# Kernel tuning notes

Measured on AMD Instinct MI355X. Metric: run time of the kernel, lower is better.

Reference implementation:

```python
import jax, jax.numpy as jnp
import numpy as np

EPS = 1e-7
CAPS_N = 1152   # 32 maps * 6 * 6
CAPS1_DIM = 8
CAPS2_N = 10
CAPS2_DIM = 16


def squash(s, axis):
    sq = jnp.sum(jnp.square(s), axis=axis, keepdims=True)
    norm = jnp.sqrt(sq + EPS)
    return (sq / (1.0 + sq)) * (s / norm)


def _conv(x, k, b, stride):
    y = jax.lax.conv_general_dilated(x, k, (stride, stride), 'VALID',
                                     dimension_numbers=('NHWC', 'HWIO', 'NHWC'))
    return jax.nn.relu(y + b)


def setup_inputs() -> dict:
    key = jax.random.key(0)
    ks = jax.random.split(key, 8)
    B = 256
    return {
        'image': jax.random.uniform(ks[0], (B, 28, 28, 1), dtype=jnp.float32),
        'target': jax.random.randint(ks[1], (B,), 0, CAPS2_N),
        'conv1_w': jax.random.normal(ks[2], (9, 9, 1, 256), jnp.float32) * 0.05,
        'conv1_b': jnp.zeros((256,), jnp.float32),
        'conv2_w': jax.random.normal(ks[3], (9, 9, 256, 256), jnp.float32) * 0.02,
        'conv2_b': jnp.zeros((256,), jnp.float32),
        'W': jax.random.normal(ks[4], (1, CAPS_N, CAPS2_N, CAPS2_DIM, CAPS1_DIM), jnp.float32) * 0.1,
        'd1_w': jax.random.normal(ks[5], (CAPS2_N * CAPS2_DIM, 512), jnp.float32) * 0.05,
        'd1_b': jnp.zeros((512,), jnp.float32),
        'd2_w': jax.random.normal(ks[6], (512, 1024), jnp.float32) * 0.04,
        'd2_b': jnp.zeros((1024,), jnp.float32),
        'd3_w': jax.random.normal(ks[7], (1024, 784), jnp.float32) * 0.03,
        'd3_b': jnp.zeros((784,), jnp.float32),
    }


def reference(image, target, conv1_w, conv1_b, conv2_w, conv2_b, W,
              d1_w, d1_b, d2_w, d2_b, d3_w, d3_b):
    B = image.shape[0]
    h = _conv(image, conv1_w, conv1_b, 1)        # [B,20,20,256]
    h = _conv(h, conv2_w, conv2_b, 2)            # [B,6,6,256]
    pc = squash(h.reshape(B, CAPS_N, CAPS1_DIM), axis=-1)  # [B,1152,8]
    # u_hat[b,n,c,j] = sum_i W[0,n,c,j,i] * pc[b,n,i]  (avoids explicit tiling)
    u_hat = jnp.einsum('ncji,bni->bncj', W[0], pc)          # [B,1152,10,16]
    # round 1: softmax of zeros over the 10 digit caps == uniform 1/10
    s1 = jnp.sum(u_hat, axis=1) * (1.0 / CAPS2_N)           # [B,10,16]
    v1 = squash(s1, axis=-1)
    # agreement uv[b,n,c] = <u_hat[b,n,c,:], v1[b,c,:]>
    uv = jnp.einsum('bncj,bcj->bnc', u_hat, v1)             # [B,1152,10]
    # round 2
    c2 = jax.nn.softmax(uv, axis=2)
    s2 = jnp.einsum('bnc,bncj->bcj', c2, u_hat)             # [B,10,16]
    v2 = squash(s2, axis=-1)                                # [B,10,16]
    norm_v2 = jnp.sqrt(jnp.sum(jnp.square(v2), axis=-1, keepdims=True) + EPS)
    norm_v2 = norm_v2[:, None, :, :, None]                  # [B,1,10,1,1]
    y_pred = jnp.squeeze(jnp.argmax(norm_v2, axis=2), axis=(1, 2))  # [B,1]
    # training path: mask by target one-hot
    mask = jax.nn.one_hot(target, CAPS2_N, dtype=v2.dtype)  # [B,10]
    masked = v2 * mask[:, :, None]                          # [B,10,16]
    flat = masked.reshape(B, 1, CAPS2_N * CAPS2_DIM)        # [B,1,160]
    h1 = jax.nn.relu(flat @ d1_w + d1_b)
    h2 = jax.nn.relu(h1 @ d2_w + d2_b)
    dec = jax.nn.sigmoid(h2 @ d3_w + d3_b)                  # [B,1,784]
    return norm_v2, y_pred, dec
```

## Files before the change

### kernel.cpp

```cpp
#include <hip/hip_runtime.h>
#include <math.h>

#define EPS 1e-7f
#define IN1_ELEMS 26214400
#define BT_ELEMS  5308416

typedef float fvec4 __attribute__((ext_vector_type(4)));
typedef short short8 __attribute__((ext_vector_type(8)));
typedef __bf16 bf16x8 __attribute__((ext_vector_type(8)));

__device__ inline unsigned short f2bf(float f){
  unsigned int u = __float_as_uint(f);
  unsigned int r = (u + 0x7fffu + ((u >> 16) & 1u)) >> 16;
  return (unsigned short)r;
}
__device__ inline float bf2f(unsigned short h){
  return __uint_as_float(((unsigned int)h) << 16);
}
__device__ inline void async16(unsigned short* dst, const unsigned short* src){
  __builtin_amdgcn_global_load_lds((const __attribute__((address_space(1))) void*)src,
                                   (__attribute__((address_space(3))) void*)dst, 16, 0, 0);
}
__device__ inline fvec4 mfma_bf16(short8 a, short8 b, fvec4 c){
  return __builtin_amdgcn_mfma_f32_16x16x32_bf16(
      __builtin_bit_cast(bf16x8, a), __builtin_bit_cast(bf16x8, b), c, 0, 0, 0);
}

__global__ __launch_bounds__(256) void wt_kernel(const float* __restrict__ w2,
    unsigned short* __restrict__ BTh, unsigned short* __restrict__ BTl){
  __shared__ float tile[64][65];
  int t = threadIdx.x;
  int k0 = blockIdx.x * 64, oc0 = blockIdx.y * 64;
  #pragma unroll
  for (int p = 0; p < 16; ++p){
    int f = p*256 + t;
    int kr = f >> 6, cc = f & 63;
    tile[kr][cc] = w2[(size_t)(k0 + kr)*256 + oc0 + cc];
  }
  __syncthreads();
  #pragma unroll
  for (int p = 0; p < 16; ++p){
    int f = p*256 + t;
    int ocr = f >> 6, kc = f & 63;
    float v = tile[kc][ocr];
    unsigned short h = f2bf(v);
    size_t idx = (size_t)(oc0 + ocr)*20736 + k0 + kc;
    BTh[idx] = h;
    BTl[idx] = f2bf(v - bf2f(h));
  }
}

__global__ __launch_bounds__(256) void conv1_kernel(const float* __restrict__ img,
    const float* __restrict__ w1, const float* __restrict__ b1,
    unsigned short* __restrict__ outh, unsigned short* __restrict__ outl){
  __shared__ float sim[252];
  int t = threadIdx.x;
  int oh = blockIdx.x, b = blockIdx.y;
  if (t < 252) sim[t] = img[((size_t)b*28 + oh + t/28)*28 + (t%28)];
  __syncthreads();
  float acc[20];
  #pragma unroll
  for (int i = 0; i < 20; ++i) acc[i] = 0.f;
  #pragma unroll
  for (int kh = 0; kh < 9; ++kh){
    float im[28];
    #pragma unroll
    for (int c = 0; c < 28; ++c) im[c] = sim[kh*28 + c];
    #pragma unroll
    for (int kw = 0; kw < 9; ++kw){
      float wv = w1[(kh*9 + kw)*256 + t];
      #pragma unroll
      for (int ow = 0; ow < 20; ++ow) acc[ow] = fmaf(im[ow + kw], wv, acc[ow]);
    }
  }
  float bv = b1[t];
  size_t base = ((size_t)(b*20 + oh))*20*256 + t;
  #pragma unroll
  for (int ow = 0; ow < 20; ++ow){
    float v = fmaxf(acc[ow] + bv, 0.f);
    unsigned short h = f2bf(v);
    outh[base + ow*256] = h;
    outl[base + ow*256] = f2bf(v - bf2f(h));
  }
}

__global__ __launch_bounds__(256) void conv2_mfma(const unsigned short* __restrict__ in1h,
    const unsigned short* __restrict__ BTh, float* __restrict__ out){
  __shared__ __align__(16) unsigned short lds[16384];
  const int t = threadIdx.x;
  const int lane = t & 63, w = t >> 6;
  const int m0 = blockIdx.y * 128, n0 = blockIdx.x * 128;
  const int rowA = t >> 2, seg = t & 3;

  const unsigned short* aS[2];
  const unsigned short* bS[2];
  #pragma unroll
  for (int h = 0; h < 2; ++h){
    int m = m0 + h*64 + rowA;
    int bb = m / 36, s = m - bb*36, oh = s / 6, ow = s - oh*6;
    aS[h] = in1h + ((size_t)((bb*20 + 2*oh)*20 + 2*ow))*256 + seg*8;
    int n = n0 + h*64 + rowA;
    bS[h] = BTh + (size_t)n*20736 + seg*8;
  }
  unsigned short* dstA = &lds[rowA*32 + seg*8];
  unsigned short* dstB = &lds[8192 + rowA*32 + seg*8];

  fvec4 acc[4][4];
  #pragma unroll
  for (int i=0;i<4;++i)
    #pragma unroll
    for (int j=0;j<4;++j) acc[i][j] = (fvec4){0.f,0.f,0.f,0.f};

  const int qm = (w >> 1)*64, qn = (w & 1)*64;
  const int ks0 = blockIdx.z * 81, ks1 = ks0 + 81;

  for (int ks = ks0; ks < ks1; ++ks){
    int kk = ks >> 3;
    int kh = kk / 9, kw = kk - kh*9;
    int aoff = (kh*20 + kw)*256 + (ks & 7)*32;
    int boff = ks*32;
    #pragma unroll
    for (int h = 0; h < 2; ++h){
      async16(dstA + h*2048,        aS[h] + aoff);
      async16(dstA + 4096 + h*2048, aS[h] + IN1_ELEMS + aoff);
      async16(dstB + h*2048,        bS[h] + boff);
      async16(dstB + 4096 + h*2048, bS[h] + BT_ELEMS + boff);
    }
    __syncthreads();
    short8 ah[4], al[4], bh[4], bl[4];
    #pragma unroll
    for (int i=0;i<4;++i){
      int ro = (qm + i*16 + (lane & 15))*32 + (lane >> 4)*8;
      ah[i] = *(const short8*)&lds[ro];
      al[i] = *(const short8*)&lds[4096 + ro];
    }
    #pragma unroll
    for (int j=0;j<4;++j){
      int ro = (qn + j*16 + (lane & 15))*32 + (lane >> 4)*8;
      bh[j] = *(const short8*)&lds[8192 + ro];
      bl[j] = *(const short8*)&lds[12288 + ro];
    }
    #pragma unroll
    for (int i=0;i<4;++i)
      #pragma unroll
      for (int j=0;j<4;++j){
        acc[i][j] = mfma_bf16(ah[i], bh[j], acc[i][j]);
        acc[i][j] = mfma_bf16(ah[i], bl[j], acc[i][j]);
        acc[i][j] = mfma_bf16(al[i], bh[j], acc[i][j]);
      }
    __syncthreads();
  }
  #pragma unroll
  for (int i=0;i<4;++i){
    int gm = m0 + qm + i*16 + ((lane >> 4) << 2);
    #pragma unroll
    for (int j=0;j<4;++j){
      int gn = n0 + qn + j*16 + (lane & 15);
      #pragma unroll
      for (int r=0;r<4;++r)
        atomicAdd(&out[(size_t)(gm + r)*256 + gn], acc[i][j][r]);
    }
  }
}

__global__ __launch_bounds__(256) void squash_pc_kernel(const float* __restrict__ c2out,
    const float* __restrict__ b2, float* __restrict__ pc){
  int g = blockIdx.x*256 + threadIdx.x;
  const float* s = c2out + (size_t)g*8;
  int oc0 = (g & 31) * 8;
  float v[8], sq = 0.f;
  #pragma unroll
  for (int e=0;e<8;++e){ float x = fmaxf(s[e] + b2[oc0+e], 0.f); v[e] = x; sq += x*x; }
  float fac = sq / ((1.f + sq) * sqrtf(sq + EPS));
  float* o = pc + (size_t)g*8;
  #pragma unroll
  for (int e=0;e<8;++e) o[e] = v[e]*fac;
}

__global__ __launch_bounds__(256) void uhat_producer(const float* __restrict__ pc,
    const float* __restrict__ Wm, float* __restrict__ uhat, float* __restrict__ s1){
  __shared__ float pcl[8192];
  int t = threadIdx.x;
  int n0 = blockIdx.x * 16, b0 = blockIdx.y * 64;
  #pragma unroll
  for (int p = 0; p < 32; ++p){
    int f = p*256 + t;
    int bl = f >> 7, rem = f & 127;
    pcl[f] = pc[((size_t)(b0 + bl)*1152 + n0)*8 + rem];
  }
  __syncthreads();
  for (int r = 0; r < 40; ++r){
    int item = r*256 + t;
    int bl = item / 160, cj = item - bl*160;
    float s1a = 0.f;
    size_t ub = ((size_t)(b0 + bl)*1152 + n0)*160 + cj;
    const float* pb = &pcl[bl*128];
    #pragma unroll 4
    for (int nl = 0; nl < 16; ++nl){
      const float4* wp = (const float4*)&Wm[((size_t)(n0 + nl)*160 + cj)*8];
      float4 w0 = wp[0], w1 = wp[1];
      const float4* pp = (const float4*)&pb[nl*8];
      float4 p0 = pp[0], p1 = pp[1];
      float uh = w0.x*p0.x + w0.y*p0.y + w0.z*p0.z + w0.w*p0.w
               + w1.x*p1.x + w1.y*p1.y + w1.z*p1.z + w1.w*p1.w;
      uhat[ub + (size_t)nl*160] = uh;
      s1a += uh;
    }
    atomicAdd(&s1[(b0 + bl)*160 + cj], s1a);
  }
}

__global__ __launch_bounds__(64) void squash_v1_kernel(const float* __restrict__ s1,
    float* __restrict__ v1){
  int g = blockIdx.x*64 + threadIdx.x;
  if (g >= 2560) return;
  const float* s = s1 + g*16;
  float x[16], sq = 0.f;
  #pragma unroll
  for (int j=0;j<16;++j){ float v = s[j]*0.1f; x[j] = v; sq += v*v; }
  float fac = sq / ((1.f + sq) * sqrtf(sq + EPS));
  float* o = v1 + g*16;
  #pragma unroll
  for (int j=0;j<16;++j) o[j] = x[j]*fac;
}

__global__ __launch_bounds__(256) void routing_kernel(const float* __restrict__ uhat,
    const float* __restrict__ v1, float* __restrict__ s2){
  __shared__ float uvl[1280];
  __shared__ float v1l[160];
  int t = threadIdx.x;
  int n0 = blockIdx.x * 128, b = blockIdx.y;
  if (t < 160) v1l[t] = v1[b*160 + t];
  __syncthreads();
  #pragma unroll
  for (int p = 0; p < 5; ++p){
    int item = p*256 + t;
    int nl = item / 10, c = item - nl*10;
    const float4* up = (const float4*)&uhat[((size_t)b*1152 + n0 + nl)*160 + c*16];
    const float* vv = &v1l[c*16];
    float4 q0 = up[0], q1 = up[1], q2 = up[2], q3 = up[3];
    float uv = q0.x*vv[0] + q0.y*vv[1] + q0.z*vv[2] + q0.w*vv[3]
             + q1.x*vv[4] + q1.y*vv[5] + q1.z*vv[6] + q1.w*vv[7]
             + q2.x*vv[8] + q2.y*vv[9] + q2.z*vv[10]+ q2.w*vv[11]
             + q3.x*vv[12]+ q3.y*vv[13]+ q3.z*vv[14]+ q3.w*vv[15];
    uvl[item] = uv;
  }
  __syncthreads();
  if (t < 128){
    float* row = &uvl[t*10];
    float mx = row[0];
    #pragma unroll
    for (int c=1;c<10;++c) mx = fmaxf(mx, row[c]);
    float e[10], sum = 0.f;
    #pragma unroll
    for (int c=0;c<10;++c){ e[c] = expf(row[c]-mx); sum += e[c]; }
    float inv = 1.f/sum;
    #pragma unroll
    for (int c=0;c<10;++c) row[c] = e[c]*inv;
  }
  __syncthreads();
  if (t < 160){
    int c = t >> 4;
    float a = 0.f;
    const float* ub = &uhat[((size_t)b*1152 + n0)*160 + t];
    for (int nl = 0; nl < 128; ++nl)
      a = fmaf(uvl[nl*10 + c], ub[(size_t)nl*160], a);
    atomicAdd(&s2[b*160 + t], a);
  }
}

__global__ __launch_bounds__(64) void finalize_kernel(const float* __restrict__ s2,
    const int* __restrict__ target, float* __restrict__ out_norm,
    float* __restrict__ out_pred, float* __restrict__ masked){
  __shared__ float v2l[160];
  __shared__ float nrm[10];
  int b = blockIdx.x, t = threadIdx.x;
  if (t < 10){
    const float* s = s2 + b*160 + t*16;
    float x[16], sq = 0.f;
    #pragma unroll
    for (int j=0;j<16;++j){ x[j] = s[j]; sq += x[j]*x[j]; }
    float fac = sq / ((1.f + sq) * sqrtf(sq + EPS));
    float n2 = 0.f;
    #pragma unroll
    for (int j=0;j<16;++j){ float v = x[j]*fac; v2l[t*16+j] = v; n2 += v*v; }
    float nr = sqrtf(n2 + EPS);
    nrm[t] = nr;
    out_norm[b*10 + t] = nr;
  }
  __syncthreads();
  if (t == 0){
    int am = 0; float bv = nrm[0];
    #pragma unroll
    for (int c=1;c<10;++c) if (nrm[c] > bv){ bv = nrm[c]; am = c; }
    out_pred[b] = (float)am;
  }
  int tg = target[b];
  #pragma unroll
  for (int p = 0; p < 3; ++p){
    int cj = p*64 + t;
    if (cj < 160) masked[b*160 + cj] = ((cj >> 4) == tg) ? v2l[cj] : 0.f;
  }
}

__global__ __launch_bounds__(256) void dec_gemm(const float* __restrict__ A,
    const float* __restrict__ B, const float* __restrict__ bias, float* __restrict__ C,
    int K, int N, int act){
  int t = threadIdx.x;
  int n = blockIdx.x*64 + (t & 63);
  int m = blockIdx.y*4 + (t >> 6);
  if (n >= N) return;
  float acc = 0.f;
  const float* a = A + (size_t)m*K;
  const float* bp = B + n;
  #pragma unroll 8
  for (int k = 0; k < K; ++k) acc = fmaf(a[k], bp[(size_t)k*N], acc);
  acc += bias[n];
  if (act == 0) acc = fmaxf(acc, 0.f);
  else acc = 1.f/(1.f + expf(-acc));
  C[(size_t)m*N + n] = acc;
}

extern "C" void kernel_launch(void* const* d_in, const int* in_sizes, int n_in,
                              void* d_out, int out_size, void* d_ws, size_t ws_size,
                              hipStream_t stream) {
  const float* image   = (const float*)d_in[0];
  const int*   target  = (const int*)d_in[1];
  const float* conv1_w = (const float*)d_in[2];
  const float* conv1_b = (const float*)d_in[3];
  const float* conv2_w = (const float*)d_in[4];
  const float* conv2_b = (const float*)d_in[5];
  const float* Wm      = (const float*)d_in[6];
  const float* d1_w    = (const float*)d_in[7];
  const float* d1_b    = (const float*)d_in[8];
  const float* d2_w    = (const float*)d_in[9];
  const float* d2_b    = (const float*)d_in[10];
  const float* d3_w    = (const float*)d_in[11];
  const float* d3_b    = (const float*)d_in[12];

  char* ws = (char*)d_ws;
  unsigned short* in1h = (unsigned short*)(ws);
  unsigned short* BTh  = (unsigned short*)(ws + 104857600);
  float* uhat   = (float*)(ws);
  float* c2out  = (float*)(ws + 126091264);
  float* pc     = (float*)(ws + 188743680);
  float* s1     = (float*)(ws + 198180864);
  float* s2     = (float*)(ws + 198344704);
  float* v1     = (float*)(ws + 198508544);
  float* masked = (float*)(ws + 198672384);
  float* h1     = (float*)(ws + 198836224);
  float* h2     = (float*)(ws + 199360512);

  float* out_norm = (float*)d_out;
  float* out_pred = out_norm + 2560;
  float* dec      = out_norm + 2816;

  wt_kernel<<<dim3(324,4),256,0,stream>>>(conv2_w, BTh, BTh + BT_ELEMS);
  conv1_kernel<<<dim3(20,256),256,0,stream>>>(image, conv1_w, conv1_b, in1h, in1h + IN1_ELEMS);
  hipMemsetAsync(c2out, 0, 9437184, stream);
  conv2_mfma<<<dim3(2,72,8),256,0,stream>>>(in1h, BTh, c2out);
  squash_pc_kernel<<<dim3(1152),256,0,stream>>>(c2out, conv2_b, pc);
  hipMemsetAsync(s1, 0, 327680, stream);
  uhat_producer<<<dim3(72,4),256,0,stream>>>(pc, Wm, uhat, s1);
  squash_v1_kernel<<<dim3(40),64,0,stream>>>(s1, v1);
  routing_kernel<<<dim3(9,256),256,0,stream>>>(uhat, v1, s2);
  finalize_kernel<<<dim3(256),64,0,stream>>>(s2, target, out_norm, out_pred, masked);
  dec_gemm<<<dim3(8,64),256,0,stream>>>(masked, d1_w, d1_b, h1, 160, 512, 0);
  dec_gemm<<<dim3(16,64),256,0,stream>>>(h1, d2_w, d2_b, h2, 512, 1024, 0);
  dec_gemm<<<dim3(13,64),256,0,stream>>>(h2, d3_w, d3_b, dec, 1024, 784, 1);
}
```

Measured before the change: 764.1 us.

## Load conv2 MFMA operands directly to registers, fold memsets and v1 squash

The conv2 MFMA loop no longer stages A/B tiles through LDS with global_load_lds and two barriers per k-step. Each wave now loads its bf16 hi/lo fragments straight from global memory into double-buffered registers, so the load for one step overlaps the MFMAs of the previous step. Separately, the two memsets are folded into the wt and squash_pc kernels, the squash_v1 kernel is merged into routing, and uhat_producer gets 4x more blocks over batch. Direct global fragment loads are uncoalesced 16-byte reads and lose LDS reuse across waves, raising global traffic and register pressure.

```diff
diff --git a/kernel.cpp b/kernel.cpp
--- a/kernel.cpp
+++ b/kernel.cpp
@@ -17,20 +17,19 @@
 __device__ inline float bf2f(unsigned short h){
   return __uint_as_float(((unsigned int)h) << 16);
 }
-__device__ inline void async16(unsigned short* dst, const unsigned short* src){
-  __builtin_amdgcn_global_load_lds((const __attribute__((address_space(1))) void*)src,
-                                   (__attribute__((address_space(3))) void*)dst, 16, 0, 0);
-}
 __device__ inline fvec4 mfma_bf16(short8 a, short8 b, fvec4 c){
   return __builtin_amdgcn_mfma_f32_16x16x32_bf16(
       __builtin_bit_cast(bf16x8, a), __builtin_bit_cast(bf16x8, b), c, 0, 0, 0);
 }
 
 __global__ __launch_bounds__(256) void wt_kernel(const float* __restrict__ w2,
-    unsigned short* __restrict__ BTh, unsigned short* __restrict__ BTl){
+    unsigned short* __restrict__ BTh, unsigned short* __restrict__ BTl,
+    float* __restrict__ c2out){
   __shared__ float tile[64][65];
   int t = threadIdx.x;
   int k0 = blockIdx.x * 64, oc0 = blockIdx.y * 64;
+  int bid = blockIdx.y*324 + blockIdx.x;
+  for (int g = bid*256 + t; g < 2359296; g += 1296*256) c2out[g] = 0.f;
   #pragma unroll
   for (int p = 0; p < 16; ++p){
     int f = p*256 + t;
@@ -86,24 +85,22 @@
 
 __global__ __launch_bounds__(256) void conv2_mfma(const unsigned short* __restrict__ in1h,
     const unsigned short* __restrict__ BTh, float* __restrict__ out){
-  __shared__ __align__(16) unsigned short lds[16384];
   const int t = threadIdx.x;
   const int lane = t & 63, w = t >> 6;
   const int m0 = blockIdx.y * 128, n0 = blockIdx.x * 128;
-  const int rowA = t >> 2, seg = t & 3;
-
-  const unsigned short* aS[2];
-  const unsigned short* bS[2];
-  #pragma unroll
-  for (int h = 0; h < 2; ++h){
-    int m = m0 + h*64 + rowA;
+  const int qm = (w >> 1)*64, qn = (w & 1)*64;
+  const int r16 = lane & 15, kseg = (lane >> 4)*8;
+
+  const unsigned short* aP[4];
+  const unsigned short* bP[4];
+  #pragma unroll
+  for (int i=0;i<4;++i){
+    int m = m0 + qm + i*16 + r16;
     int bb = m / 36, s = m - bb*36, oh = s / 6, ow = s - oh*6;
-    aS[h] = in1h + ((size_t)((bb*20 + 2*oh)*20 + 2*ow))*256 + seg*8;
-    int n = n0 + h*64 + rowA;
-    bS[h] = BTh + (size_t)n*20736 + seg*8;
-  }
-  unsigned short* dstA = &lds[rowA*32 + seg*8];
-  unsigned short* dstB = &lds[8192 + rowA*32 + seg*8];
+    aP[i] = in1h + ((size_t)((bb*20 + 2*oh)*20 + 2*ow))*256 + kseg;
+    int n = n0 + qn + i*16 + r16;
+    bP[i] = BTh + (size_t)n*20736 + kseg;
+  }
 
   fvec4 acc[4][4];
   #pragma unroll
@@ -111,45 +108,41 @@
     #pragma unroll
     for (int j=0;j<4;++j) acc[i][j] = (fvec4){0.f,0.f,0.f,0.f};
 
-  const int qm = (w >> 1)*64, qn = (w & 1)*64;
-  const int ks0 = blockIdx.z * 81, ks1 = ks0 + 81;
-
-  for (int ks = ks0; ks < ks1; ++ks){
-    int kk = ks >> 3;
-    int kh = kk / 9, kw = kk - kh*9;
-    int aoff = (kh*20 + kw)*256 + (ks & 7)*32;
-    int boff = ks*32;
-    #pragma unroll
-    for (int h = 0; h < 2; ++h){
-      async16(dstA + h*2048,        aS[h] + aoff);
-      async16(dstA + 4096 + h*2048, aS[h] + IN1_ELEMS + aoff);
-      async16(dstB + h*2048,        bS[h] + boff);
-      async16(dstB + 4096 + h*2048, bS[h] + BT_ELEMS + boff);
-    }
-    __syncthreads();
-    short8 ah[4], al[4], bh[4], bl[4];
-    #pragma unroll
-    for (int i=0;i<4;++i){
-      int ro = (qm + i*16 + (lane & 15))*32 + (lane >> 4)*8;
-      ah[i] = *(const short8*)&lds[ro];
-      al[i] = *(const short8*)&lds[4096 + ro];
-    }
-    #pragma unroll
-    for (int j=0;j<4;++j){
-      int ro = (qn + j*16 + (lane & 15))*32 + (lane >> 4)*8;
-      bh[j] = *(const short8*)&lds[8192 + ro];
-      bl[j] = *(const short8*)&lds[12288 + ro];
-    }
-    #pragma unroll
-    for (int i=0;i<4;++i)
-      #pragma unroll
-      for (int j=0;j<4;++j){
-        acc[i][j] = mfma_bf16(ah[i], bh[j], acc[i][j]);
-        acc[i][j] = mfma_bf16(ah[i], bl[j], acc[i][j]);
-        acc[i][j] = mfma_bf16(al[i], bh[j], acc[i][j]);
-      }
-    __syncthreads();
-  }
+  short8 ahA[4], alA[4], bhA[4], blA[4];
+  short8 ahB[4], alB[4], bhB[4], blB[4];
+
+  #define LOADSET(AH,AL,BH,BL,KS) do{                                   \
+    int kk_ = (KS) >> 3; int kh_ = kk_/9, kw_ = kk_ - kh_*9;            \
+    int aoff_ = (kh_*20 + kw_)*256 + ((KS) & 7)*32;                     \
+    int boff_ = (KS)*32;                                                \
+    _Pragma("unroll")                                                   \
+    for (int i_=0;i_<4;++i_){                                           \
+      AH[i_] = *(const short8*)(aP[i_] + aoff_);                        \
+      AL[i_] = *(const short8*)(aP[i_] + IN1_ELEMS + aoff_);            \
+      BH[i_] = *(const short8*)(bP[i_] + boff_);                        \
+      BL[i_] = *(const short8*)(bP[i_] + BT_ELEMS + boff_);             \
+    } }while(0)
+
+  #define COMPUTE(AH,AL,BH,BL) do{                                      \
+    _Pragma("unroll")                                                   \
+    for (int i_=0;i_<4;++i_)                                            \
+      _Pragma("unroll")                                                 \
+      for (int j_=0;j_<4;++j_){                                         \
+        acc[i_][j_] = mfma_bf16(AH[i_], BH[j_], acc[i_][j_]);           \
+        acc[i_][j_] = mfma_bf16(AH[i_], BL[j_], acc[i_][j_]);           \
+        acc[i_][j_] = mfma_bf16(AL[i_], BH[j_], acc[i_][j_]);           \
+      } }while(0)
+
+  const int ks0 = blockIdx.z * 81;
+  LOADSET(ahA,alA,bhA,blA, ks0);
+  for (int ks = ks0; ks < ks0 + 80; ks += 2){
+    LOADSET(ahB,alB,bhB,blB, ks+1);
+    COMPUTE(ahA,alA,bhA,blA);
+    LOADSET(ahA,alA,bhA,blA, ks+2);
+    COMPUTE(ahB,alB,bhB,blB);
+  }
+  COMPUTE(ahA,alA,bhA,blA);
+
   #pragma unroll
   for (int i=0;i<4;++i){
     int gm = m0 + qm + i*16 + ((lane >> 4) << 2);
@@ -164,8 +157,9 @@
 }
 
 __global__ __launch_bounds__(256) void squash_pc_kernel(const float* __restrict__ c2out,
-    const float* __restrict__ b2, float* __restrict__ pc){
+    const float* __restrict__ b2, float* __restrict__ pc, float* __restrict__ s1s2){
   int g = blockIdx.x*256 + threadIdx.x;
+  if (g < 81920) s1s2[g] = 0.f;
   const float* s = c2out + (size_t)g*8;
   int oc0 = (g & 31) * 8;
   float v[8], sq = 0.f;
@@ -179,17 +173,17 @@
 
 __global__ __launch_bounds__(256) void uhat_producer(const float* __restrict__ pc,
     const float* __restrict__ Wm, float* __restrict__ uhat, float* __restrict__ s1){
-  __shared__ float pcl[8192];
-  int t = threadIdx.x;
-  int n0 = blockIdx.x * 16, b0 = blockIdx.y * 64;
-  #pragma unroll
-  for (int p = 0; p < 32; ++p){
+  __shared__ float pcl[2048];
+  int t = threadIdx.x;
+  int n0 = blockIdx.x * 16, b0 = blockIdx.y * 16;
+  #pragma unroll
+  for (int p = 0; p < 8; ++p){
     int f = p*256 + t;
     int bl = f >> 7, rem = f & 127;
     pcl[f] = pc[((size_t)(b0 + bl)*1152 + n0)*8 + rem];
   }
   __syncthreads();
-  for (int r = 0; r < 40; ++r){
+  for (int r = 0; r < 10; ++r){
     int item = r*256 + t;
     int bl = item / 160, cj = item - bl*160;
     float s1a = 0.f;
@@ -210,27 +204,22 @@
   }
 }
 
-__global__ __launch_bounds__(64) void squash_v1_kernel(const float* __restrict__ s1,
-    float* __restrict__ v1){
-  int g = blockIdx.x*64 + threadIdx.x;
-  if (g >= 2560) return;
-  const float* s = s1 + g*16;
-  float x[16], sq = 0.f;
-  #pragma unroll
-  for (int j=0;j<16;++j){ float v = s[j]*0.1f; x[j] = v; sq += v*v; }
-  float fac = sq / ((1.f + sq) * sqrtf(sq + EPS));
-  float* o = v1 + g*16;
-  #pragma unroll
-  for (int j=0;j<16;++j) o[j] = x[j]*fac;
-}
-
 __global__ __launch_bounds__(256) void routing_kernel(const float* __restrict__ uhat,
-    const float* __restrict__ v1, float* __restrict__ s2){
+    const float* __restrict__ s1, float* __restrict__ s2){
   __shared__ float uvl[1280];
   __shared__ float v1l[160];
+  __shared__ float facl[10];
   int t = threadIdx.x;
   int n0 = blockIdx.x * 128, b = blockIdx.y;
-  if (t < 160) v1l[t] = v1[b*160 + t];
+  if (t < 10){
+    const float* s = s1 + b*160 + t*16;
+    float sq = 0.f;
+    #pragma unroll
+    for (int j=0;j<16;++j){ float v = s[j]*0.1f; sq += v*v; }
+    facl[t] = 0.1f * sq / ((1.f + sq) * sqrtf(sq + EPS));
+  }
+  __syncthreads();
+  if (t < 160) v1l[t] = s1[b*160 + t] * facl[t >> 4];
   __syncthreads();
   #pragma unroll
   for (int p = 0; p < 5; ++p){
@@ -346,7 +335,6 @@
   float* pc     = (float*)(ws + 188743680);
   float* s1     = (float*)(ws + 198180864);
   float* s2     = (float*)(ws + 198344704);
-  float* v1     = (float*)(ws + 198508544);
   float* masked = (float*)(ws + 198672384);
   float* h1     = (float*)(ws + 198836224);
   float* h2     = (float*)(ws + 199360512);
@@ -355,15 +343,12 @@
   float* out_pred = out_norm + 2560;
   float* dec      = out_norm + 2816;
 
-  wt_kernel<<<dim3(324,4),256,0,stream>>>(conv2_w, BTh, BTh + BT_ELEMS);
+  wt_kernel<<<dim3(324,4),256,0,stream>>>(conv2_w, BTh, BTh + BT_ELEMS, c2out);
   conv1_kernel<<<dim3(20,256),256,0,stream>>>(image, conv1_w, conv1_b, in1h, in1h + IN1_ELEMS);
-  hipMemsetAsync(c2out, 0, 9437184, stream);
   conv2_mfma<<<dim3(2,72,8),256,0,stream>>>(in1h, BTh, c2out);
-  squash_pc_kernel<<<dim3(1152),256,0,stream>>>(c2out, conv2_b, pc);
-  hipMemsetAsync(s1, 0, 327680, stream);
-  uhat_producer<<<dim3(72,4),256,0,stream>>>(pc, Wm, uhat, s1);
-  squash_v1_kernel<<<dim3(40),64,0,stream>>>(s1, v1);
-  routing_kernel<<<dim3(9,256),256,0,stream>>>(uhat, v1, s2);
+  squash_pc_kernel<<<dim3(1152),256,0,stream>>>(c2out, conv2_b, pc, s1);
+  uhat_producer<<<dim3(72,16),256,0,stream>>>(pc, Wm, uhat, s1);
+  routing_kernel<<<dim3(9,256),256,0,stream>>>(uhat, s1, s2);
   finalize_kernel<<<dim3(256),64,0,stream>>>(s2, target, out_norm, out_pred, masked);
   dec_gemm<<<dim3(8,64),256,0,stream>>>(masked, d1_w, d1_b, h1, 160, 512, 0);
   dec_gemm<<<dim3(16,64),256,0,stream>>>(h1, d2_w, d2_b, h2, 512, 1024, 0);
```

Result: slower. 1.116 ms (+46.1%).

## Fragment-order LDS layout for conv2, fuse memsets and v1 squash, regrid uhat

Applied to the files above, without the earlier changes.

The conv2 MFMA kernel now writes global-to-LDS loads in MFMA fragment order, so each lane reads a contiguous 16 bytes, and it adds a launch-bounds occupancy hint. The two memsets are folded into wt_kernel and squash_pc_kernel. The v1 squash is recomputed inside routing_kernel, removing a launch. uhat_producer uses 16 batches per block for a larger grid. The aim is fewer launches and fewer LDS bank conflicts; the risk is that s2 is zeroed while squash_pc also writes and reads other data, which depends on buffer ordering.

```diff
diff --git a/kernel.cpp b/kernel.cpp
--- a/kernel.cpp
+++ b/kernel.cpp
@@ -27,10 +27,13 @@
 }
 
 __global__ __launch_bounds__(256) void wt_kernel(const float* __restrict__ w2,
-    unsigned short* __restrict__ BTh, unsigned short* __restrict__ BTl){
+    unsigned short* __restrict__ BTh, unsigned short* __restrict__ BTl,
+    float* __restrict__ c2out){
   __shared__ float tile[64][65];
   int t = threadIdx.x;
   int k0 = blockIdx.x * 64, oc0 = blockIdx.y * 64;
+  int bid = blockIdx.y*324 + blockIdx.x;
+  for (int g = bid*256 + t; g < 2359296; g += 1296*256) c2out[g] = 0.f;
   #pragma unroll
   for (int p = 0; p < 16; ++p){
     int f = p*256 + t;
@@ -84,26 +87,26 @@
   }
 }
 
-__global__ __launch_bounds__(256) void conv2_mfma(const unsigned short* __restrict__ in1h,
+__global__ __launch_bounds__(256,3) void conv2_mfma(const unsigned short* __restrict__ in1h,
     const unsigned short* __restrict__ BTh, float* __restrict__ out){
   __shared__ __align__(16) unsigned short lds[16384];
   const int t = threadIdx.x;
   const int lane = t & 63, w = t >> 6;
   const int m0 = blockIdx.y * 128, n0 = blockIdx.x * 128;
-  const int rowA = t >> 2, seg = t & 3;
+  const int r16 = t & 15, q = (t >> 4) & 3;
 
   const unsigned short* aS[2];
   const unsigned short* bS[2];
   #pragma unroll
   for (int h = 0; h < 2; ++h){
-    int m = m0 + h*64 + rowA;
+    int m = m0 + h*64 + w*16 + r16;
     int bb = m / 36, s = m - bb*36, oh = s / 6, ow = s - oh*6;
-    aS[h] = in1h + ((size_t)((bb*20 + 2*oh)*20 + 2*ow))*256 + seg*8;
-    int n = n0 + h*64 + rowA;
-    bS[h] = BTh + (size_t)n*20736 + seg*8;
-  }
-  unsigned short* dstA = &lds[rowA*32 + seg*8];
-  unsigned short* dstB = &lds[8192 + rowA*32 + seg*8];
+    aS[h] = in1h + ((size_t)((bb*20 + 2*oh)*20 + 2*ow))*256 + q*8;
+    int n = n0 + h*64 + w*16 + r16;
+    bS[h] = BTh + (size_t)n*20736 + q*8;
+  }
+  unsigned short* dstA = &lds[t*8];
+  unsigned short* dstB = &lds[8192 + t*8];
 
   fvec4 acc[4][4];
   #pragma unroll
@@ -111,7 +114,7 @@
     #pragma unroll
     for (int j=0;j<4;++j) acc[i][j] = (fvec4){0.f,0.f,0.f,0.f};
 
-  const int qm = (w >> 1)*64, qn = (w & 1)*64;
+  const int tm = (w >> 1)*4, tn = (w & 1)*4;
   const int ks0 = blockIdx.z * 81, ks1 = ks0 + 81;
 
   for (int ks = ks0; ks < ks1; ++ks){
@@ -130,15 +133,15 @@
     short8 ah[4], al[4], bh[4], bl[4];
     #pragma unroll
     for (int i=0;i<4;++i){
-      int ro = (qm + i*16 + (lane & 15))*32 + (lane >> 4)*8;
+      int ro = (tm + i)*512 + lane*8;
       ah[i] = *(const short8*)&lds[ro];
       al[i] = *(const short8*)&lds[4096 + ro];
     }
     #pragma unroll
     for (int j=0;j<4;++j){
-      int ro = (qn + j*16 + (lane & 15))*32 + (lane >> 4)*8;
-      bh[j] = *(const short8*)&lds[8192 + ro];
-      bl[j] = *(const short8*)&lds[12288 + ro];
+      int rn = (tn + j)*512 + lane*8;
+      bh[j] = *(const short8*)&lds[8192 + rn];
+      bl[j] = *(const short8*)&lds[12288 + rn];
     }
     #pragma unroll
     for (int i=0;i<4;++i)
@@ -150,6 +153,7 @@
       }
     __syncthreads();
   }
+  const int qm = (w >> 1)*64, qn = (w & 1)*64;
   #pragma unroll
   for (int i=0;i<4;++i){
     int gm = m0 + qm + i*16 + ((lane >> 4) << 2);
@@ -164,8 +168,9 @@
 }
 
 __global__ __launch_bounds__(256) void squash_pc_kernel(const float* __restrict__ c2out,
-    const float* __restrict__ b2, float* __restrict__ pc){
+    const float* __restrict__ b2, float* __restrict__ pc, float* __restrict__ s1s2){
   int g = blockIdx.x*256 + threadIdx.x;
+  if (g < 81920) s1s2[g] = 0.f;
   const float* s = c2out + (size_t)g*8;
   int oc0 = (g & 31) * 8;
   float v[8], sq = 0.f;
@@ -179,17 +184,17 @@
 
 __global__ __launch_bounds__(256) void uhat_producer(const float* __restrict__ pc,
     const float* __restrict__ Wm, float* __restrict__ uhat, float* __restrict__ s1){
-  __shared__ float pcl[8192];
-  int t = threadIdx.x;
-  int n0 = blockIdx.x * 16, b0 = blockIdx.y * 64;
-  #pragma unroll
-  for (int p = 0; p < 32; ++p){
+  __shared__ float pcl[2048];
+  int t = threadIdx.x;
+  int n0 = blockIdx.x * 16, b0 = blockIdx.y * 16;
+  #pragma unroll
+  for (int p = 0; p < 8; ++p){
     int f = p*256 + t;
     int bl = f >> 7, rem = f & 127;
     pcl[f] = pc[((size_t)(b0 + bl)*1152 + n0)*8 + rem];
   }
   __syncthreads();
-  for (int r = 0; r < 40; ++r){
+  for (int r = 0; r < 10; ++r){
     int item = r*256 + t;
     int bl = item / 160, cj = item - bl*160;
     float s1a = 0.f;
@@ -210,27 +215,22 @@
   }
 }
 
-__global__ __launch_bounds__(64) void squash_v1_kernel(const float* __restrict__ s1,
-    float* __restrict__ v1){
-  int g = blockIdx.x*64 + threadIdx.x;
-  if (g >= 2560) return;
-  const float* s = s1 + g*16;
-  float x[16], sq = 0.f;
-  #pragma unroll
-  for (int j=0;j<16;++j){ float v = s[j]*0.1f; x[j] = v; sq += v*v; }
-  float fac = sq / ((1.f + sq) * sqrtf(sq + EPS));
-  float* o = v1 + g*16;
-  #pragma unroll
-  for (int j=0;j<16;++j) o[j] = x[j]*fac;
-}
-
 __global__ __launch_bounds__(256) void routing_kernel(const float* __restrict__ uhat,
-    const float* __restrict__ v1, float* __restrict__ s2){
+    const float* __restrict__ s1, float* __restrict__ s2){
   __shared__ float uvl[1280];
   __shared__ float v1l[160];
+  __shared__ float facl[10];
   int t = threadIdx.x;
   int n0 = blockIdx.x * 128, b = blockIdx.y;
-  if (t < 160) v1l[t] = v1[b*160 + t];
+  if (t < 10){
+    const float* s = s1 + b*160 + t*16;
+    float sq = 0.f;
+    #pragma unroll
+    for (int j=0;j<16;++j){ float v = s[j]*0.1f; sq += v*v; }
+    facl[t] = 0.1f * sq / ((1.f + sq) * sqrtf(sq + EPS));
+  }
+  __syncthreads();
+  if (t < 160) v1l[t] = s1[b*160 + t] * facl[t >> 4];
   __syncthreads();
   #pragma unroll
   for (int p = 0; p < 5; ++p){
@@ -346,7 +346,6 @@
   float* pc     = (float*)(ws + 188743680);
   float* s1     = (float*)(ws + 198180864);
   float* s2     = (float*)(ws + 198344704);
-  float* v1     = (float*)(ws + 198508544);
   float* masked = (float*)(ws + 198672384);
   float* h1     = (float*)(ws + 198836224);
   float* h2     = (float*)(ws + 199360512);
@@ -355,15 +354,12 @@
   float* out_pred = out_norm + 2560;
   float* dec      = out_norm + 2816;
 
-  wt_kernel<<<dim3(324,4),256,0,stream>>>(conv2_w, BTh, BTh + BT_ELEMS);
+  wt_kernel<<<dim3(324,4),256,0,stream>>>(conv2_w, BTh, BTh + BT_ELEMS, c2out);
   conv1_kernel<<<dim3(20,256),256,0,stream>>>(image, conv1_w, conv1_b, in1h, in1h + IN1_ELEMS);
-  hipMemsetAsync(c2out, 0, 9437184, stream);
   conv2_mfma<<<dim3(2,72,8),256,0,stream>>>(in1h, BTh, c2out);
-  squash_pc_kernel<<<dim3(1152),256,0,stream>>>(c2out, conv2_b, pc);
-  hipMemsetAsync(s1, 0, 327680, stream);
-  uhat_producer<<<dim3(72,4),256,0,stream>>>(pc, Wm, uhat, s1);
-  squash_v1_kernel<<<dim3(40),64,0,stream>>>(s1, v1);
-  routing_kernel<<<dim3(9,256),256,0,stream>>>(uhat, v1, s2);
+  squash_pc_kernel<<<dim3(1152),256,0,stream>>>(c2out, conv2_b, pc, s1);
+  uhat_producer<<<dim3(72,16),256,0,stream>>>(pc, Wm, uhat, s1);
+  routing_kernel<<<dim3(9,256),256,0,stream>>>(uhat, s1, s2);
   finalize_kernel<<<dim3(256),64,0,stream>>>(s2, target, out_norm, out_pred, masked);
   dec_gemm<<<dim3(8,64),256,0,stream>>>(masked, d1_w, d1_b, h1, 160, 512, 0);
   dec_gemm<<<dim3(16,64),256,0,stream>>>(h1, d2_w, d2_b, h2, 512, 1024, 0);
```

After: 795.5 us. +4.1%, slower.
